# Performance work log

Hardware: AMD Instinct MI355X
Metric: run time of the kernel (lower is better)

Reference implementation:

```python
import jax, jax.numpy as jnp
import numpy as np

K, N, D, NCONV, E = 3, 30000, 128, 6, 480000


def _graph_conv(x, src, dst, ew, Wp, bp, Wrel, Wroot):
    # SAGE-style project=True: pre-project+relu source features
    h = jax.nn.relu(x @ Wp + bp)                    # [N, D]
    msg = ew[:, None] * h[src]                      # [E, D] gather
    agg = jax.ops.segment_sum(msg, dst, num_segments=N)
    cnt = jax.ops.segment_sum(jnp.ones_like(ew), dst, num_segments=N)
    agg = agg / jnp.maximum(cnt, 1.0)[:, None]      # mean aggregation
    return agg @ Wrel + x @ Wroot                   # GraphConv: lin_rel(agg)+lin_root(x), bias=False


def setup_inputs() -> dict:
    key = jax.random.key(0)
    ks = jax.random.split(key, 16)
    w = lambda k, s: (jax.random.normal(k, s, jnp.float32) * 0.05)
    inp = {
        "H_K_prev": jax.random.normal(ks[0], (K, N, D), jnp.float32),
        "edgelists": jax.random.randint(ks[1], (K, 2, E), 0, N, jnp.int32),
        "spec_weight": jax.random.uniform(ks[2], (K, NCONV, E), jnp.float32),
        # 6 stacked GraphConv params
        "Wp": w(ks[3], (NCONV, D, D)),
        "bp": jnp.zeros((NCONV, D), jnp.float32),
        "Wrel": w(ks[4], (NCONV, D, D)),
        "Wroot": w(ks[5], (NCONV, D, D)),
        # combine projection (7D -> 3D) and proj_linear (4D -> D)
        "W_comb": w(ks[6], ((NCONV + 1) * D, 3 * D)),
        "b_comb": jnp.zeros((3 * D,), jnp.float32),
        "W_pl": w(ks[7], (4 * D, D)),
        "b_pl": jnp.zeros((D,), jnp.float32),
        # LSTM (torch gate order i,f,g,o)
        "Wih": w(ks[8], (4 * D, D)),
        "Whh": w(ks[9], (4 * D, D)),
        "bih": jnp.zeros((4 * D,), jnp.float32),
        "bhh": jnp.zeros((4 * D,), jnp.float32),
    }
    return inp


def reference(H_K_prev, edgelists, spec_weight, Wp, bp, Wrel, Wroot,
              W_comb, b_comb, W_pl, b_pl, Wih, Whh, bih, bhh):
    outs = []
    for k in range(K):  # fixed small history loop
        Hk = H_K_prev[k]
        src, dst = edgelists[k, 0], edgelists[k, 1]
        feats = [Hk] + [
            _graph_conv(Hk, src, dst, spec_weight[k, i],
                        Wp[i], bp[i], Wrel[i], Wroot[i])
            for i in range(NCONV)
        ]
        cat = jnp.concatenate(feats, axis=1)               # [N, 7D]
        proj = jax.nn.relu(cat @ W_comb + b_comb)          # [N, 3D] (dropout=eval identity)
        outs.append(jnp.concatenate([Hk, proj], axis=1) @ W_pl + b_pl)  # [N, D]
    xs = jnp.stack(outs, 0)                                # [K, N, D] time-major

    def cell(carry, x_t):
        h, c = carry
        gates = x_t @ Wih.T + h @ Whh.T + bih + bhh        # [N, 4D]
        i, f, g, o = jnp.split(gates, 4, axis=1)
        c = jax.nn.sigmoid(f) * c + jax.nn.sigmoid(i) * jnp.tanh(g)
        h = jax.nn.sigmoid(o) * jnp.tanh(c)
        return (h, c), None

    z = jnp.zeros((N, D), xs.dtype)
    (h, _), _ = jax.lax.scan(cell, (z, z), xs)
    return jax.nn.relu(h)[None]                            # [1, N, D]
```

## Files before the change

kernel.cpp:

```cpp
#include <hip/hip_runtime.h>
#include <math.h>

constexpr int NN  = 30000;
constexpr int DIM = 128;
constexpr int KH  = 3;
constexpr int NC  = 6;
constexpr int EE  = 480000;
constexpr int NBLK3 = (3 * NN + 255) / 256;

typedef __attribute__((ext_vector_type(8))) short short8;
typedef __attribute__((ext_vector_type(4))) float f32x4;
typedef __attribute__((ext_vector_type(2))) float f32x2;

__device__ __forceinline__ unsigned short f2bf(float f) {
    union { float f; unsigned int i; } c; c.f = f;
    unsigned int u = c.i;
    return (unsigned short)((u + 0x7fffu + ((u >> 16) & 1u)) >> 16);
}
__device__ __forceinline__ float bf2f(unsigned int u) {
    union { unsigned int i; float f; } c; c.i = u << 16; return c.f;
}
__device__ __forceinline__ unsigned int packbf(float x, float y) {
    return (unsigned int)f2bf(x) | ((unsigned int)f2bf(y) << 16);
}
__device__ __forceinline__ float fsig(float x) {
    return __builtin_amdgcn_rcpf(1.f + __expf(-x));
}
__device__ __forceinline__ float ftanh(float x) {
    return 2.f * fsig(2.f * x) - 1.f;
}

template<int OUT, bool RELU>
__global__ __launch_bounds__(256) void mgemm(
    const unsigned short* __restrict__ A1, int lda1,
    const unsigned short* __restrict__ A2, int lda2, int ksplit,
    const unsigned short* __restrict__ Bt, int ldb,
    const float* __restrict__ bias,
    void* __restrict__ Cv, int ldc,
    int M, int K, int nx)
{
    __shared__ __align__(16) unsigned char smem[2 * 128 * 80];
    unsigned char* As = smem;
    unsigned char* Bs = smem + 128 * 80;

    const int nwg  = gridDim.x;
    const int orig = blockIdx.x;
    const int q = nwg >> 3, r = nwg & 7;
    const int xcd = orig & 7, idx = orig >> 3;
    const int lin = (xcd < r ? xcd * (q + 1) : r * (q + 1) + (xcd - r) * q) + idx;
    const int bx = lin % nx, by = lin / nx;

    const int tid  = threadIdx.x;
    const int lane = tid & 63;
    const int w    = tid >> 6;
    const int wm   = w >> 1, wn = w & 1;
    const int lm   = lane & 15, lg = lane >> 4;
    const int bm   = by * 128;
    const int bn   = bx * 128;

    const int srow  = tid >> 1;
    const int shalf = tid & 1;

    f32x4 acc[4][4] = {};

    int arow = bm + srow; if (arow > M - 1) arow = M - 1;
    const int brow = bn + srow;

    for (int k0 = 0; k0 < K; k0 += 32) {
        const unsigned short* Ap; int la; int kk;
        if (k0 < ksplit) { Ap = A1; la = lda1; kk = k0; }
        else             { Ap = A2; la = lda2; kk = k0 - ksplit; }
        const float4* ga = (const float4*)(Ap + (size_t)arow * la + kk + shalf * 16);
        float4 a0 = ga[0], a1 = ga[1];
        const float4* gb = (const float4*)(Bt + (size_t)brow * ldb + k0 + shalf * 16);
        float4 b0 = gb[0], b1 = gb[1];

        __syncthreads();
        *(float4*)(As + srow * 80 + shalf * 32)      = a0;
        *(float4*)(As + srow * 80 + shalf * 32 + 16) = a1;
        *(float4*)(Bs + srow * 80 + shalf * 32)      = b0;
        *(float4*)(Bs + srow * 80 + shalf * 32 + 16) = b1;
        __syncthreads();

        short8 av[4], bv[4];
        #pragma unroll
        for (int f = 0; f < 4; ++f) {
            av[f] = *(const short8*)(As + (wm * 64 + f * 16 + lm) * 80 + lg * 16);
            bv[f] = *(const short8*)(Bs + (wn * 64 + f * 16 + lm) * 80 + lg * 16);
        }
        #pragma unroll
        for (int i = 0; i < 4; ++i)
            #pragma unroll
            for (int j = 0; j < 4; ++j)
                acc[i][j] = __builtin_amdgcn_mfma_f32_16x16x32_bf16(
                    av[i], bv[j], acc[i][j], 0, 0, 0);
    }

    #pragma unroll
    for (int i = 0; i < 4; ++i) {
        int row0 = bm + wm * 64 + i * 16 + lg * 4;
        #pragma unroll
        for (int j = 0; j < 4; ++j) {
            int col = bn + wn * 64 + j * 16 + lm;
            float bb = bias[col];
            #pragma unroll
            for (int r2 = 0; r2 < 4; ++r2) {
                int row = row0 + r2;
                if (row < M) {
                    float v = acc[i][j][r2] + bb;
                    if (RELU) v = fmaxf(v, 0.f);
                    if (OUT == 0) {
                        ((unsigned short*)Cv)[(size_t)row * ldc + col] = f2bf(v);
                    } else {
                        unsigned int pk = __builtin_amdgcn_cvt_pk_fp8_f32(v, v, 0, false);
                        ((unsigned char*)Cv)[(size_t)row * ldc + col] = (unsigned char)pk;
                    }
                }
            }
        }
    }
}

__global__ void hist3(const int* __restrict__ EL, int* __restrict__ cnt)
{
    int t = blockIdx.x * 256 + threadIdx.x;
    int e0 = t * 4;
    if (e0 >= 3 * EE) return;
    int g = e0 / EE;
    int e = e0 - g * EE;
    int4 d4 = *(const int4*)(EL + (size_t)g * 2 * EE + EE + e);
    int* c = cnt + g * NN;
    atomicAdd(&c[d4.x], 1);
    atomicAdd(&c[d4.y], 1);
    atomicAdd(&c[d4.z], 1);
    atomicAdd(&c[d4.w], 1);
}

__global__ __launch_bounds__(256) void scan_part(const int* __restrict__ cnt,
                                                 int* __restrict__ off,
                                                 int* __restrict__ bsum, int n)
{
    int lane = threadIdx.x & 63, wid = threadIdx.x >> 6;
    int i = blockIdx.x * 256 + threadIdx.x;
    int v = (i < n) ? cnt[i] : 0;
    int x = v;
    #pragma unroll
    for (int ofs = 1; ofs < 64; ofs <<= 1) {
        int t = __shfl_up(x, ofs, 64);
        if (lane >= ofs) x += t;
    }
    __shared__ int ws[4];
    if (lane == 63) ws[wid] = x;
    __syncthreads();
    int wo = 0;
    for (int j = 0; j < wid; ++j) wo += ws[j];
    if (i < n) off[i] = wo + x - v;
    if (threadIdx.x == 255) bsum[blockIdx.x] = wo + x;
}

__global__ __launch_bounds__(512) void scan_tops(const int* __restrict__ bsum,
                                                 int* __restrict__ btop, int nb)
{
    __shared__ int buf[512];
    int v = (threadIdx.x < nb) ? bsum[threadIdx.x] : 0;
    buf[threadIdx.x] = v;
    __syncthreads();
    #pragma unroll
    for (int ofs = 1; ofs < 512; ofs <<= 1) {
        int t = (threadIdx.x >= ofs) ? buf[threadIdx.x - ofs] : 0;
        __syncthreads();
        buf[threadIdx.x] += t;
        __syncthreads();
    }
    if (threadIdx.x < nb) btop[threadIdx.x] = buf[threadIdx.x] - v;
}

__global__ __launch_bounds__(256) void scan_add(int* __restrict__ off,
                                                const int* __restrict__ btop,
                                                int* __restrict__ cursor,
                                                int n, int etot)
{
    int i = blockIdx.x * 256 + threadIdx.x;
    if (i < n) {
        int o = off[i] + btop[blockIdx.x];
        off[i] = o;
        cursor[i] = o;
    }
    if (blockIdx.x == 0 && threadIdx.x == 0) off[n] = etot;
}

__global__ void fill3(const int* __restrict__ EL, const float* __restrict__ SW,
                      int* __restrict__ cursor, uint4* __restrict__ rec)
{
    int t = blockIdx.x * 256 + threadIdx.x;
    int e0 = t * 4;
    if (e0 >= 3 * EE) return;
    int g = e0 / EE;
    int e = e0 - g * EE;
    const int* base = EL + (size_t)g * 2 * EE;
    int4 s4 = *(const int4*)(base + e);
    int4 d4 = *(const int4*)(base + EE + e);
    const float* sw = SW + (size_t)g * NC * EE;
    float4 w0 = *(const float4*)(sw + e);
    float4 w1 = *(const float4*)(sw + (size_t)EE + e);
    float4 w2 = *(const float4*)(sw + 2 * (size_t)EE + e);
    float4 w3 = *(const float4*)(sw + 3 * (size_t)EE + e);
    float4 w4 = *(const float4*)(sw + 4 * (size_t)EE + e);
    float4 w5 = *(const float4*)(sw + 5 * (size_t)EE + e);
    int* cur = cursor + g * NN;
    int p0 = atomicAdd(&cur[d4.x], 1);
    int p1 = atomicAdd(&cur[d4.y], 1);
    int p2 = atomicAdd(&cur[d4.z], 1);
    int p3 = atomicAdd(&cur[d4.w], 1);
    rec[p0] = make_uint4((unsigned)s4.x, packbf(w0.x, w1.x), packbf(w2.x, w3.x), packbf(w4.x, w5.x));
    rec[p1] = make_uint4((unsigned)s4.y, packbf(w0.y, w1.y), packbf(w2.y, w3.y), packbf(w4.y, w5.y));
    rec[p2] = make_uint4((unsigned)s4.z, packbf(w0.z, w1.z), packbf(w2.z, w3.z), packbf(w4.z, w5.z));
    rec[p3] = make_uint4((unsigned)s4.w, packbf(w0.w, w1.w), packbf(w2.w, w3.w), packbf(w4.w, w5.w));
}

__device__ __forceinline__ void wunpack(uint4 r, int half,
                                        float& w0, float& w1, float& w2)
{
    if (half == 0) {
        w0 = bf2f(r.y & 0xffffu); w1 = bf2f(r.y >> 16); w2 = bf2f(r.z & 0xffffu);
    } else {
        w0 = bf2f(r.z >> 16); w1 = bf2f(r.w & 0xffffu); w2 = bf2f(r.w >> 16);
    }
}

__global__ __launch_bounds__(256) void gather6(
    const unsigned char* __restrict__ h8,
    const uint4* __restrict__ rec,
    const int* __restrict__ off,
    unsigned short* __restrict__ agg)
{
    int wid  = threadIdx.x >> 6;
    int lane = threadIdx.x & 63;
    int node = blockIdx.x * 2 + (wid >> 1);
    int half = wid & 1;
    if (node >= NN) return;
    int s0 = off[node], s1 = off[node + 1];
    float a0 = 0.f, a1 = 0.f, b0 = 0.f, b1 = 0.f, c0 = 0.f, c1 = 0.f;
    const size_t hofs = (size_t)half * 384 + (size_t)lane * 2;

    int e = s0;
    for (; e + 3 < s1; e += 4) {
        uint4 rA = rec[e], rB = rec[e + 1], rC = rec[e + 2], rD = rec[e + 3];
        const unsigned short* pA = (const unsigned short*)(h8 + (size_t)rA.x * 768 + hofs);
        const unsigned short* pB = (const unsigned short*)(h8 + (size_t)rB.x * 768 + hofs);
        const unsigned short* pC = (const unsigned short*)(h8 + (size_t)rC.x * 768 + hofs);
        const unsigned short* pD = (const unsigned short*)(h8 + (size_t)rD.x * 768 + hofs);
        unsigned int pA0 = pA[0], pA1 = pA[64], pA2 = pA[128];
        unsigned int pB0 = pB[0], pB1 = pB[64], pB2 = pB[128];
        unsigned int pC0 = pC[0], pC1 = pC[64], pC2 = pC[128];
        unsigned int pD0 = pD[0], pD1 = pD[64], pD2 = pD[128];

        float w0, w1, w2;
        wunpack(rA, half, w0, w1, w2);
        {
            f32x2 h0 = __builtin_amdgcn_cvt_pk_f32_fp8(pA0, false);
            f32x2 h1 = __builtin_amdgcn_cvt_pk_f32_fp8(pA1, false);
            f32x2 h2 = __builtin_amdgcn_cvt_pk_f32_fp8(pA2, false);
            a0 += w0 * h0.x; a1 += w0 * h0.y;
            b0 += w1 * h1.x; b1 += w1 * h1.y;
            c0 += w2 * h2.x; c1 += w2 * h2.y;
        }
        wunpack(rB, half, w0, w1, w2);
        {
            f32x2 h0 = __builtin_amdgcn_cvt_pk_f32_fp8(pB0, false);
            f32x2 h1 = __builtin_amdgcn_cvt_pk_f32_fp8(pB1, false);
            f32x2 h2 = __builtin_amdgcn_cvt_pk_f32_fp8(pB2, false);
            a0 += w0 * h0.x; a1 += w0 * h0.y;
            b0 += w1 * h1.x; b1 += w1 * h1.y;
            c0 += w2 * h2.x; c1 += w2 * h2.y;
        }
        wunpack(rC, half, w0, w1, w2);
        {
            f32x2 h0 = __builtin_amdgcn_cvt_pk_f32_fp8(pC0, false);
            f32x2 h1 = __builtin_amdgcn_cvt_pk_f32_fp8(pC1, false);
            f32x2 h2 = __builtin_amdgcn_cvt_pk_f32_fp8(pC2, false);
            a0 += w0 * h0.x; a1 += w0 * h0.y;
            b0 += w1 * h1.x; b1 += w1 * h1.y;
            c0 += w2 * h2.x; c1 += w2 * h2.y;
        }
        wunpack(rD, half, w0, w1, w2);
        {
            f32x2 h0 = __builtin_amdgcn_cvt_pk_f32_fp8(pD0, false);
            f32x2 h1 = __builtin_amdgcn_cvt_pk_f32_fp8(pD1, false);
            f32x2 h2 = __builtin_amdgcn_cvt_pk_f32_fp8(pD2, false);
            a0 += w0 * h0.x; a1 += w0 * h0.y;
            b0 += w1 * h1.x; b1 += w1 * h1.y;
            c0 += w2 * h2.x; c1 += w2 * h2.y;
        }
    }
    for (; e < s1; ++e) {
        uint4 r = rec[e];
        float w0, w1, w2;
        wunpack(r, half, w0, w1, w2);
        const unsigned short* hrow = (const unsigned short*)(h8 + (size_t)r.x * 768 + hofs);
        unsigned int p0 = hrow[0];
        unsigned int p1 = hrow[64];
        unsigned int p2 = hrow[128];
        f32x2 h0 = __builtin_amdgcn_cvt_pk_f32_fp8(p0, false);
        f32x2 h1 = __builtin_amdgcn_cvt_pk_f32_fp8(p1, false);
        f32x2 h2 = __builtin_amdgcn_cvt_pk_f32_fp8(p2, false);
        a0 += w0 * h0.x; a1 += w0 * h0.y;
        b0 += w1 * h1.x; b1 += w1 * h1.y;
        c0 += w2 * h2.x; c1 += w2 * h2.y;
    }
    float inv = 1.f / fmaxf((float)(s1 - s0), 1.f);
    unsigned int* orow = (unsigned int*)(agg + (size_t)node * 768) + 192 * half + lane;
    orow[0]   = packbf(a0 * inv, a1 * inv);
    orow[64]  = packbf(b0 * inv, b1 * inv);
    orow[128] = packbf(c0 * inv, c1 * inv);
}

__global__ void cvt_h(const float* __restrict__ Hk, unsigned int* __restrict__ out,
                      int total)
{
    int idx = blockIdx.x * 256 + threadIdx.x;
    if (idx >= total) return;
    float2 v = ((const float2*)Hk)[idx];
    out[idx] = packbf(v.x, v.y);
}

#define SWA32(r, b) ((r) * 512 + ((b) ^ (((r) & 7) << 4)))

__global__ __launch_bounds__(512) void lstm_fused(
    const unsigned short* __restrict__ xs,
    const unsigned short* __restrict__ Wt,
    const float* __restrict__ bsum,
    float* __restrict__ outp)
{
    __shared__ __align__(16) unsigned char AL[32 * 512];

    const int tid  = threadIdx.x;
    const int lane = tid & 63;
    const int w    = tid >> 6;
    const int lm   = lane & 15, lg = lane >> 4;
    const int node0 = blockIdx.x * 32;

    float bias[4];
    #pragma unroll
    for (int g = 0; g < 4; ++g)
        bias[g] = bsum[w * 64 + g * 16 + lm];

    short8 bw[8][4];
    #pragma unroll
    for (int ks = 0; ks < 8; ++ks)
        #pragma unroll
        for (int g = 0; g < 4; ++g)
            bw[ks][g] = *(const short8*)(Wt +
                (size_t)(w * 64 + g * 16 + lm) * 256 + ks * 32 + lg * 8);

    float cst[2][4] = {};

    float4 z4 = make_float4(0.f, 0.f, 0.f, 0.f);
    {
        int r = tid >> 4, gi = tid & 15;
        *(float4*)(AL + SWA32(r, 256 + gi * 16)) = z4;
    }

    for (int t = 0; t < KH; ++t) {
        const unsigned short* xsrc = xs + (size_t)t * NN * 128;
        {
            int r = tid >> 4, gi = tid & 15;
            int gr = node0 + r; if (gr >= NN) gr = NN - 1;
            float4 v = *(const float4*)(xsrc + (size_t)gr * 128 + gi * 8);
            *(float4*)(AL + SWA32(r, gi * 16)) = v;
        }
        __syncthreads();

        f32x4 acc[2][4] = {};
        #pragma unroll
        for (int ks = 0; ks < 8; ++ks) {
            short8 av[2];
            #pragma unroll
            for (int i = 0; i < 2; ++i)
                av[i] = *(const short8*)(AL + SWA32(i * 16 + lm, ks * 64 + lg * 16));
            #pragma unroll
            for (int g = 0; g < 4; ++g)
                #pragma unroll
                for (int i = 0; i < 2; ++i)
                    acc[i][g] = __builtin_amdgcn_mfma_f32_16x16x32_bf16(
                        av[i], bw[ks][g], acc[i][g], 0, 0, 0);
        }
        __syncthreads();

        #pragma unroll
        for (int i = 0; i < 2; ++i)
            #pragma unroll
            for (int r = 0; r < 4; ++r) {
                float giv = acc[i][0][r] + bias[0];
                float gfv = acc[i][1][r] + bias[1];
                float ggv = acc[i][2][r] + bias[2];
                float gov = acc[i][3][r] + bias[3];
                float si = fsig(giv);
                float sf = fsig(gfv);
                float so = fsig(gov);
                float cv = sf * cst[i][r] + si * ftanh(ggv);
                cst[i][r] = cv;
                float hv = so * ftanh(cv);
                int row = i * 16 + lg * 4 + r;
                int d   = w * 16 + lm;
                if (t < KH - 1) {
                    *(unsigned short*)(AL + SWA32(row, 256 + 2 * d)) = f2bf(hv);
                } else if (node0 + row < NN) {
                    outp[(size_t)(node0 + row) * 128 + d] = fmaxf(hv, 0.f);
                }
            }
    }
}

__global__ __launch_bounds__(256) void wt_fold(
    const float* __restrict__ Wcomb,
    const float* __restrict__ Wroot,
    const float* __restrict__ Wrel,
    unsigned short* __restrict__ Wfull_t)
{
    __shared__ __align__(16) float As[16][68];
    __shared__ __align__(16) float Bs[16][68];
    const int tid = threadIdx.x;
    const int tx = tid & 15, ty = tid >> 4;
    const int bm = blockIdx.y * 64;
    const int bn = blockIdx.x * 64;
    const bool root = (bm < 128);
    const int i0 = root ? 0 : (bm >> 7) - 1;
    const int i1 = root ? NC : i0 + 1;
    const int mloc = bm & 127;
    const int a_m = tid >> 2, a_k = (tid & 3) * 4;
    const int b_k = tid >> 4, b_n = (tid & 15) * 4;

    float acc[4][4] = {};

    for (int i = i0; i < i1; ++i) {
        const float* A = (root ? Wroot : Wrel) + (size_t)i * 128 * 128;
        const float* B = Wcomb + (size_t)(i + 1) * 128 * 384;
        for (int k0 = 0; k0 < 128; k0 += 16) {
            float4 va = *(const float4*)(A + (size_t)(mloc + a_m) * 128 + k0 + a_k);
            float4 vb = *(const float4*)(B + (size_t)(k0 + b_k) * 384 + bn + b_n);
            __syncthreads();
            As[a_k + 0][a_m] = va.x; As[a_k + 1][a_m] = va.y;
            As[a_k + 2][a_m] = va.z; As[a_k + 3][a_m] = va.w;
            *(float4*)&Bs[b_k][b_n] = vb;
            __syncthreads();
            #pragma unroll
            for (int kk = 0; kk < 16; ++kk) {
                float4 av = *(const float4*)&As[kk][ty * 4];
                float4 bv = *(const float4*)&Bs[kk][tx * 4];
                float a[4] = {av.x, av.y, av.z, av.w};
                float b[4] = {bv.x, bv.y, bv.z, bv.w};
                #pragma unroll
                for (int ii = 0; ii < 4; ++ii)
                    #pragma unroll
                    for (int j = 0; j < 4; ++j)
                        acc[ii][j] += a[ii] * b[j];
            }
        }
    }

    #pragma unroll
    for (int ii = 0; ii < 4; ++ii) {
        int m = bm + ty * 4 + ii;
        #pragma unroll
        for (int j = 0; j < 4; ++j) {
            int n = bn + tx * 4 + j;
            float v = acc[ii][j];
            if (root) v += Wcomb[(size_t)m * 384 + n];
            Wfull_t[(size_t)n * 896 + m] = f2bf(v);
        }
    }
}

__global__ __launch_bounds__(256) void tr_cvt(
    const float* __restrict__ src, unsigned short* __restrict__ dst,
    int R, int C)
{
    __shared__ float s[32][33];
    const float* sb = src + (size_t)blockIdx.z * R * C;
    unsigned short* db = dst + (size_t)blockIdx.z * R * C;
    int r0 = blockIdx.y * 32, c0 = blockIdx.x * 32;
    int tx = threadIdx.x & 31, ty = threadIdx.x >> 5;
    #pragma unroll
    for (int q = 0; q < 4; ++q)
        s[ty + q * 8][tx] = sb[(size_t)(r0 + ty + q * 8) * C + c0 + tx];
    __syncthreads();
    #pragma unroll
    for (int q = 0; q < 4; ++q)
        db[(size_t)(c0 + ty + q * 8) * R + r0 + tx] = f2bf(s[tx][ty + q * 8]);
}

__global__ void wt_lstm(const float* __restrict__ Wih, const float* __restrict__ Whh,
                        const float* __restrict__ bih, const float* __restrict__ bhh,
                        unsigned short* __restrict__ Wt, float* __restrict__ bsum)
{
    int idx = blockIdx.x * 256 + threadIdx.x;
    if (idx < 512) {
        int w = idx >> 6, rem = idx & 63, g = rem >> 4, d16 = rem & 15;
        int n = g * 128 + w * 16 + d16;
        bsum[idx] = bih[n] + bhh[n];
    }
    if (idx >= 512 * 256) return;
    int k = idx & 255, np = idx >> 8;
    int w = np >> 6, rem = np & 63, g = rem >> 4, d16 = rem & 15;
    int n = g * 128 + w * 16 + d16;
    Wt[idx] = f2bf(k < 128 ? Wih[(size_t)n * DIM + k]
                           : Whh[(size_t)n * DIM + (k - 128)]);
}

extern "C" void kernel_launch(void* const* d_in, const int* in_sizes, int n_in,
                              void* d_out, int out_size, void* d_ws, size_t ws_size,
                              hipStream_t stream)
{
    const float* H     = (const float*)d_in[0];
    const int*   EL    = (const int*)  d_in[1];
    const float* SW    = (const float*)d_in[2];
    const float* Wp    = (const float*)d_in[3];
    const float* bp    = (const float*)d_in[4];
    const float* Wrel  = (const float*)d_in[5];
    const float* Wroot = (const float*)d_in[6];
    const float* Wcomb = (const float*)d_in[7];
    const float* bcomb = (const float*)d_in[8];
    const float* Wpl   = (const float*)d_in[9];
    const float* bpl   = (const float*)d_in[10];
    const float* Wih   = (const float*)d_in[11];
    const float* Whh   = (const float*)d_in[12];
    const float* bih   = (const float*)d_in[13];
    const float* bhh   = (const float*)d_in[14];

    char* wp = (char*)d_ws;
    auto alloc = [&](size_t b) {
        char* p = wp; wp += (b + 255) & ~(size_t)255; return p;
    };
    unsigned short* Hbf  = (unsigned short*)alloc((size_t)3 * NN * 128 * 2);
    unsigned char*  h8   = (unsigned char*) alloc((size_t)NN * 768);
    unsigned short* agg  = (unsigned short*)alloc((size_t)NN * 768 * 2);
    unsigned short* proj = (unsigned short*)alloc((size_t)NN * 384 * 2);
    unsigned short* xs   = (unsigned short*)alloc((size_t)KH * NN * 128 * 2);
    int* cnt     = (int*)alloc((size_t)3 * NN * 4);
    int* off     = (int*)alloc((size_t)(3 * NN + 1) * 4);
    int* cursor  = (int*)alloc((size_t)3 * NN * 4);
    int* bsum    = (int*)alloc((size_t)NBLK3 * 4);
    int* btop    = (int*)alloc((size_t)NBLK3 * 4);
    uint4* rec   = (uint4*)alloc((size_t)3 * EE * 16);
    unsigned short* Wp_t     = (unsigned short*)alloc((size_t)768 * 128 * 2);
    unsigned short* Wfull_t  = (unsigned short*)alloc((size_t)384 * 896 * 2);
    unsigned short* Wpl_t    = (unsigned short*)alloc((size_t)128 * 512 * 2);
    unsigned short* WihWhh_t = (unsigned short*)alloc((size_t)512 * 256 * 2);
    float* bias_lstm         = (float*)alloc(512 * 4);

    tr_cvt<<<dim3(4, 4, 6), 256, 0, stream>>>(Wp, Wp_t, 128, 128);
    wt_fold<<<dim3(6, 14), 256, 0, stream>>>(Wcomb, Wroot, Wrel, Wfull_t);
    tr_cvt<<<dim3(4, 16, 1), 256, 0, stream>>>(Wpl, Wpl_t, 512, 128);
    wt_lstm<<<(512 * 256 + 255) / 256, 256, 0, stream>>>(Wih, Whh, bih, bhh,
                                                         WihWhh_t, bias_lstm);

    hipMemsetAsync(cnt, 0, (size_t)3 * NN * 4, stream);
    hist3<<<(3 * EE / 4 + 255) / 256, 256, 0, stream>>>(EL, cnt);
    scan_part<<<NBLK3, 256, 0, stream>>>(cnt, off, bsum, 3 * NN);
    scan_tops<<<1, 512, 0, stream>>>(bsum, btop, NBLK3);
    scan_add<<<NBLK3, 256, 0, stream>>>(off, btop, cursor, 3 * NN, 3 * EE);
    fill3<<<(3 * EE / 4 + 255) / 256, 256, 0, stream>>>(EL, SW, cursor, rec);

    cvt_h<<<(3 * NN * 64 + 255) / 256, 256, 0, stream>>>(H, (unsigned int*)Hbf,
                                                         3 * NN * 64);

    const int MB = (NN + 127) / 128;

    for (int k = 0; k < KH; ++k) {
        const unsigned short* Hbk = Hbf + (size_t)k * NN * 128;

        mgemm<1, true><<<6 * MB, 256, 0, stream>>>(
            Hbk, 128, (const unsigned short*)nullptr, 0, 128,
            Wp_t, 128, bp, h8, 768, NN, 128, 6);

        gather6<<<NN / 2, 256, 0, stream>>>(h8, rec, off + k * NN, agg);

        mgemm<0, true><<<3 * MB, 256, 0, stream>>>(
            Hbk, 128, agg, 768, 128,
            Wfull_t, 896, bcomb, proj, 384, NN, 896, 3);

        mgemm<0, false><<<1 * MB, 256, 0, stream>>>(
            Hbk, 128, proj, 384, 128,
            Wpl_t, 512, bpl, xs + (size_t)k * NN * 128, 128, NN, 512, 1);
    }

    lstm_fused<<<(NN + 31) / 32, 512, 0, stream>>>(xs, WihWhh_t, bias_lstm,
                                                   (float*)d_out);
}
```

Measured before the change: 747.0 us.

## Replace per-node atomic CSR fill with two-pass bucketed counting sort

The CSR edge-record build no longer does a global atomicAdd per destination node with scattered 16-byte writes. Edges are first scattered into 32-node buckets whose padded cursors sit on separate cache lines. A per-bucket block then places each record at its final position using shared-memory atomics. This aims to cut global atomic contention and scatter traffic, at the cost of an extra 23 MB temp buffer, an extra full pass over the records, and two more kernel launches.

```diff
diff --git a/kernel.cpp b/kernel.cpp
--- a/kernel.cpp
+++ b/kernel.cpp
@@ -7,6 +7,8 @@
 constexpr int NC  = 6;
 constexpr int EE  = 480000;
 constexpr int NBLK3 = (3 * NN + 255) / 256;
+constexpr int NBKT  = (NN + 31) / 32;
+constexpr int NBKT3 = 3 * NBKT;
 
 typedef __attribute__((ext_vector_type(8))) short short8;
 typedef __attribute__((ext_vector_type(4))) float f32x4;
@@ -177,45 +179,62 @@
 
 __global__ __launch_bounds__(256) void scan_add(int* __restrict__ off,
                                                 const int* __restrict__ btop,
-                                                int* __restrict__ cursor,
                                                 int n, int etot)
 {
     int i = blockIdx.x * 256 + threadIdx.x;
-    if (i < n) {
-        int o = off[i] + btop[blockIdx.x];
-        off[i] = o;
-        cursor[i] = o;
-    }
+    if (i < n) off[i] += btop[blockIdx.x];
     if (blockIdx.x == 0 && threadIdx.x == 0) off[n] = etot;
 }
 
-__global__ void fill3(const int* __restrict__ EL, const float* __restrict__ SW,
-                      int* __restrict__ cursor, uint4* __restrict__ rec)
+__global__ void bcur_init(const int* __restrict__ off, int* __restrict__ bcur16)
 {
     int t = blockIdx.x * 256 + threadIdx.x;
-    int e0 = t * 4;
-    if (e0 >= 3 * EE) return;
-    int g = e0 / EE;
-    int e = e0 - g * EE;
+    if (t >= NBKT3) return;
+    int g = t / NBKT, lb = t - g * NBKT;
+    bcur16[t * 16] = off[g * NN + lb * 32];
+}
+
+__global__ void fill_bucket(const int* __restrict__ EL, const float* __restrict__ SW,
+                            int* __restrict__ bcur16, uint4* __restrict__ tmp)
+{
+    int i = blockIdx.x * 256 + threadIdx.x;
+    if (i >= 3 * EE) return;
+    int g = i / EE;
+    int e = i - g * EE;
     const int* base = EL + (size_t)g * 2 * EE;
-    int4 s4 = *(const int4*)(base + e);
-    int4 d4 = *(const int4*)(base + EE + e);
+    int src = base[e], dst = base[EE + e];
     const float* sw = SW + (size_t)g * NC * EE;
-    float4 w0 = *(const float4*)(sw + e);
-    float4 w1 = *(const float4*)(sw + (size_t)EE + e);
-    float4 w2 = *(const float4*)(sw + 2 * (size_t)EE + e);
-    float4 w3 = *(const float4*)(sw + 3 * (size_t)EE + e);
-    float4 w4 = *(const float4*)(sw + 4 * (size_t)EE + e);
-    float4 w5 = *(const float4*)(sw + 5 * (size_t)EE + e);
-    int* cur = cursor + g * NN;
-    int p0 = atomicAdd(&cur[d4.x], 1);
-    int p1 = atomicAdd(&cur[d4.y], 1);
-    int p2 = atomicAdd(&cur[d4.z], 1);
-    int p3 = atomicAdd(&cur[d4.w], 1);
-    rec[p0] = make_uint4((unsigned)s4.x, packbf(w0.x, w1.x), packbf(w2.x, w3.x), packbf(w4.x, w5.x));
-    rec[p1] = make_uint4((unsigned)s4.y, packbf(w0.y, w1.y), packbf(w2.y, w3.y), packbf(w4.y, w5.y));
-    rec[p2] = make_uint4((unsigned)s4.z, packbf(w0.z, w1.z), packbf(w2.z, w3.z), packbf(w4.z, w5.z));
-    rec[p3] = make_uint4((unsigned)s4.w, packbf(w0.w, w1.w), packbf(w2.w, w3.w), packbf(w4.w, w5.w));
+    int b = g * NBKT + (dst >> 5);
+    int pos = atomicAdd(&bcur16[b * 16], 1);
+    uint4 rv;
+    rv.x = (unsigned)src | ((unsigned)(dst & 31) << 15);
+    rv.y = packbf(sw[e],                  sw[(size_t)EE + e]);
+    rv.z = packbf(sw[2 * (size_t)EE + e], sw[3 * (size_t)EE + e]);
+    rv.w = packbf(sw[4 * (size_t)EE + e], sw[5 * (size_t)EE + e]);
+    tmp[pos] = rv;
+}
+
+__global__ __launch_bounds__(256) void sort_bucket(const uint4* __restrict__ tmp,
+                                                   const int* __restrict__ off,
+                                                   uint4* __restrict__ rec)
+{
+    __shared__ int lcnt[32];
+    int b = blockIdx.x;
+    int g = b / NBKT, lb = b - g * NBKT;
+    int n0 = lb * 32;
+    int gn0 = g * NN + n0;
+    int ncnt = NN - n0; if (ncnt > 32) ncnt = 32;
+    int bstart = off[gn0], bend = off[gn0 + ncnt];
+    if (threadIdx.x < 32) lcnt[threadIdx.x] = 0;
+    __syncthreads();
+    for (int i = bstart + (int)threadIdx.x; i < bend; i += 256) {
+        uint4 r = tmp[i];
+        int d = (r.x >> 15) & 31;
+        int rank = atomicAdd(&lcnt[d], 1);
+        int fin = off[gn0 + d] + rank;
+        r.x &= 0x7fffu;
+        rec[fin] = r;
+    }
 }
 
 __device__ __forceinline__ void wunpack(uint4 r, int half,
@@ -539,9 +558,10 @@
     unsigned short* xs   = (unsigned short*)alloc((size_t)KH * NN * 128 * 2);
     int* cnt     = (int*)alloc((size_t)3 * NN * 4);
     int* off     = (int*)alloc((size_t)(3 * NN + 1) * 4);
-    int* cursor  = (int*)alloc((size_t)3 * NN * 4);
     int* bsum    = (int*)alloc((size_t)NBLK3 * 4);
     int* btop    = (int*)alloc((size_t)NBLK3 * 4);
+    int* bcur16  = (int*)alloc((size_t)NBKT3 * 16 * 4);
+    uint4* tmp   = (uint4*)alloc((size_t)3 * EE * 16);
     uint4* rec   = (uint4*)alloc((size_t)3 * EE * 16);
     unsigned short* Wp_t     = (unsigned short*)alloc((size_t)768 * 128 * 2);
     unsigned short* Wfull_t  = (unsigned short*)alloc((size_t)384 * 896 * 2);
@@ -559,8 +579,10 @@
     hist3<<<(3 * EE / 4 + 255) / 256, 256, 0, stream>>>(EL, cnt);
     scan_part<<<NBLK3, 256, 0, stream>>>(cnt, off, bsum, 3 * NN);
     scan_tops<<<1, 512, 0, stream>>>(bsum, btop, NBLK3);
-    scan_add<<<NBLK3, 256, 0, stream>>>(off, btop, cursor, 3 * NN, 3 * EE);
-    fill3<<<(3 * EE / 4 + 255) / 256, 256, 0, stream>>>(EL, SW, cursor, rec);
+    scan_add<<<NBLK3, 256, 0, stream>>>(off, btop, 3 * NN, 3 * EE);
+    bcur_init<<<(NBKT3 + 255) / 256, 256, 0, stream>>>(off, bcur16);
+    fill_bucket<<<(3 * EE + 255) / 256, 256, 0, stream>>>(EL, SW, bcur16, tmp);
+    sort_bucket<<<NBKT3, 256, 0, stream>>>(tmp, off, rec);
 
     cvt_h<<<(3 * NN * 64 + 255) / 256, 256, 0, stream>>>(H, (unsigned int*)Hbf,
                                                          3 * NN * 64);
```

Result: no change. 757.5 us (+1.4%).
